# Kernel tuning notes

Measured on AMD Instinct MI355X. Metric: run time of the kernel, lower is better.

Reference implementation:

```python
import jax, jax.numpy as jnp
import numpy as np

N = 50000      # nodes
E = 800000     # edges (before self-loops)
F_IN = 128     # raw node feature dim
D = 500        # GCN_in_dim = gcn_dim = h_mlp_dim
T = 200000     # number of triplets


def setup_inputs() -> dict:
    key = jax.random.key(0)
    ks = jax.random.split(key, 13)
    s = 0.05
    return {
        "feats": jax.random.normal(ks[0], (N, F_IN), jnp.float32),
        "W_aff": jax.random.normal(ks[1], (F_IN, D), jnp.float32) * s,
        "b_aff": jax.random.normal(ks[2], (D,), jnp.float32) * s,
        "W_gcn": jax.random.normal(ks[3], (D, D), jnp.float32) * s,
        "b_gcn": jax.random.normal(ks[4], (D,), jnp.float32) * s,
        "W_pred_in": jax.random.normal(ks[5], (2 * D, D), jnp.float32) * s,
        "b_pred_in": jax.random.normal(ks[6], (D,), jnp.float32) * s,
        "W_pred_out": jax.random.normal(ks[7], (D, 1), jnp.float32) * s,
        "b_pred_out": jax.random.normal(ks[8], (1,), jnp.float32) * s,
        "src": jax.random.randint(ks[9], (E,), 0, N),
        "dst": jax.random.randint(ks[10], (E,), 0, N),
        "triplets": jax.random.randint(ks[11], (T, 3), 0, N),
    }


def reference(feats, W_aff, b_aff, W_gcn, b_gcn, W_pred_in, b_pred_in,
              W_pred_out, b_pred_out, src, dst, triplets):
    n = feats.shape[0]
    # LinearAffine (use_pre_linearAffine=True)
    x = feats @ W_aff + b_aff                      # [N, D]

    # dgl.add_self_loop
    loop = jnp.arange(n)
    s_idx = jnp.concatenate([src, loop])
    d_idx = jnp.concatenate([dst, loop])

    # GraphConv, norm='both', no edge weights, activation=None
    ones = jnp.ones(s_idx.shape[0], jnp.float32)
    out_deg = jax.ops.segment_sum(ones, s_idx, num_segments=n)
    in_deg = jax.ops.segment_sum(ones, d_idx, num_segments=n)
    norm_src = jnp.where(out_deg > 0, jax.lax.rsqrt(out_deg), 0.0)  # [N]
    norm_dst = jnp.where(in_deg > 0, jax.lax.rsqrt(in_deg), 0.0)    # [N]

    xw = x @ W_gcn                                  # [N, D]
    msg = xw[s_idx] * norm_src[s_idx, None]         # [E+N, D] gather
    agg = jax.ops.segment_sum(msg, d_idx, num_segments=n)  # scatter-add
    embedding = agg * norm_dst[:, None] + b_gcn     # [N, D]

    # triplet gather + MLP_edge_predictor (layer_num=2: cat->Linear->Linear)
    s_feat = embedding[triplets[:, 0]]              # [T, D]
    o_feat = embedding[triplets[:, 2]]              # [T, D]
    t = jnp.concatenate([s_feat, o_feat], axis=-1) @ W_pred_in + b_pred_in
    weights = t @ W_pred_out + b_pred_out           # [T, 1]
    return (weights, embedding)
```

## Files before the change

### kernel.cpp

```cpp
#include <hip/hip_runtime.h>


typedef float f32x4 __attribute__((ext_vector_type(4)));
typedef short s16x8 __attribute__((ext_vector_type(8)));

__device__ __forceinline__ unsigned short f2bf(float f) {
    unsigned u = __float_as_uint(f);
    unsigned r = (u + 0x7FFFu + ((u >> 16) & 1u)) >> 16;
    return (unsigned short)r;
}

__device__ __forceinline__ void async_ld16(const void* g, void* lds) {
    __builtin_amdgcn_global_load_lds(
        (const __attribute__((address_space(1))) unsigned int*)g,
        (__attribute__((address_space(3))) unsigned int*)lds,
        16, 0, 0);
}

__global__ __launch_bounds__(256) void init_kernel(
    unsigned* __restrict__ gpad, int nG,
    float* __restrict__ hpad, int nH, int* __restrict__ bh, int nB) {
    const int stride = gridDim.x * blockDim.x;
    const int i0 = blockIdx.x * blockDim.x + threadIdx.x;
    for (int i = i0; i < nG; i += stride) gpad[i] = 0u;
    for (int i = i0; i < nH; i += stride) hpad[i] = 0.f;
    for (int i = i0; i < nB; i += stride) bh[i] = 0;
}

__global__ __launch_bounds__(256) void hist2_kernel(
    const int* __restrict__ src, const int* __restrict__ dst,
    int* __restrict__ bhist_src, int* __restrict__ bhist_dst, int E) {
    __shared__ int lhs[256], lhd[256];
    lhs[threadIdx.x] = 0;
    lhd[threadIdx.x] = 0;
    __syncthreads();
    const int stride = gridDim.x * blockDim.x;
    for (int e = blockIdx.x * blockDim.x + threadIdx.x; e < E; e += stride) {
        atomicAdd(&lhs[src[e] >> 8], 1);
        atomicAdd(&lhd[dst[e] >> 8], 1);
    }
    __syncthreads();
    int cs = lhs[threadIdx.x], cd = lhd[threadIdx.x];
    if (cs > 0) atomicAdd(&bhist_src[threadIdx.x], cs);
    if (cd > 0) atomicAdd(&bhist_dst[threadIdx.x], cd);
}

__global__ void bscan2_kernel(const int* __restrict__ bhist_src, const int* __restrict__ bhist_dst,
                              int* __restrict__ sbbase, int* __restrict__ sbcursor,
                              int* __restrict__ dbbase, int* __restrict__ dbcursor,
                              int nbuk, int E) {
    __shared__ int sv[256];
    const int tid = threadIdx.x;

    int c = (tid < nbuk) ? bhist_src[tid] : 0;
    sv[tid] = c;
    __syncthreads();
    for (int st = 1; st < 256; st <<= 1) {
        int t = (tid >= st) ? sv[tid - st] : 0;
        __syncthreads();
        sv[tid] += t;
        __syncthreads();
    }
    if (tid < nbuk) { int ex = sv[tid] - c; sbbase[tid] = ex; sbcursor[tid] = ex; }
    if (tid == 0) sbbase[nbuk] = E;
    __syncthreads();

    c = (tid < nbuk) ? bhist_dst[tid] : 0;
    sv[tid] = c;
    __syncthreads();
    for (int st = 1; st < 256; st <<= 1) {
        int t = (tid >= st) ? sv[tid - st] : 0;
        __syncthreads();
        sv[tid] += t;
        __syncthreads();
    }
    if (tid < nbuk) { int ex = sv[tid] - c; dbbase[tid] = ex; dbcursor[tid] = ex; }
    if (tid == 0) dbbase[nbuk] = E;
}

#define PCH 4096
__global__ __launch_bounds__(256) void fused_partition_kernel(
    const int* __restrict__ src, const int* __restrict__ dst,
    int* __restrict__ dcursor, unsigned long long* __restrict__ pairs,
    int* __restrict__ scursor, int* __restrict__ ssorted,
    int E, int nbuk) {
    __shared__ int lhist[256];
    __shared__ int lbase[256];
    __shared__ int gbase[256];
    __shared__ int scanv[256];
    __shared__ unsigned long long lpair[PCH];
    __shared__ unsigned char lbid[PCH];

    const int tid = threadIdx.x;
    const int c0 = blockIdx.x * PCH;
    int cnt = E - c0; if (cnt > PCH) cnt = PCH;

    int dv[16], sv[16], rk[16];

    lhist[tid] = 0;
    __syncthreads();
#pragma unroll
    for (int q = 0; q < 16; ++q) {
        int e = c0 + q * 256 + tid;
        if (e < E) {
            int d = dst[e];
            dv[q] = d;
            sv[q] = src[e];
            rk[q] = atomicAdd(&lhist[d >> 8], 1);
        } else {
            dv[q] = -1;
            sv[q] = -1;
        }
    }
    __syncthreads();

    int c = lhist[tid];
    scanv[tid] = c;
    __syncthreads();
    for (int st = 1; st < 256; st <<= 1) {
        int t = (tid >= st) ? scanv[tid - st] : 0;
        __syncthreads();
        scanv[tid] += t;
        __syncthreads();
    }
    lbase[tid] = scanv[tid] - c;
    if (tid < nbuk && c > 0) gbase[tid] = atomicAdd(&dcursor[tid], c);
    __syncthreads();

#pragma unroll
    for (int q = 0; q < 16; ++q) {
        if (dv[q] >= 0) {
            int b = dv[q] >> 8;
            int slot = lbase[b] + rk[q];
            lpair[slot] = ((unsigned long long)(unsigned)dv[q] << 32) | (unsigned)sv[q];
            lbid[slot] = (unsigned char)b;
        }
    }
    __syncthreads();

    for (int i = tid; i < cnt; i += 256) {
        int b = lbid[i];
        pairs[(long)gbase[b] + (i - lbase[b])] = lpair[i];
    }
    __syncthreads();

    int* lval = (int*)lpair;
    lhist[tid] = 0;
    __syncthreads();
#pragma unroll
    for (int q = 0; q < 16; ++q) {
        if (sv[q] >= 0) rk[q] = atomicAdd(&lhist[sv[q] >> 8], 1);
    }
    __syncthreads();

    c = lhist[tid];
    scanv[tid] = c;
    __syncthreads();
    for (int st = 1; st < 256; st <<= 1) {
        int t = (tid >= st) ? scanv[tid - st] : 0;
        __syncthreads();
        scanv[tid] += t;
        __syncthreads();
    }
    lbase[tid] = scanv[tid] - c;
    if (tid < nbuk && c > 0) gbase[tid] = atomicAdd(&scursor[tid], c);
    __syncthreads();

#pragma unroll
    for (int q = 0; q < 16; ++q) {
        if (sv[q] >= 0) {
            int b = sv[q] >> 8;
            int slot = lbase[b] + rk[q];
            lval[slot] = sv[q];
            lbid[slot] = (unsigned char)b;
        }
    }
    __syncthreads();

    for (int i = tid; i < cnt; i += 256) {
        int b = lbid[i];
        ssorted[(long)gbase[b] + (i - lbase[b])] = lval[i];
    }
}

__global__ __launch_bounds__(256) void bucket_finalize_kernel(
    const unsigned long long* __restrict__ pairs, const int* __restrict__ dbbase,
    const int* __restrict__ ssorted, const int* __restrict__ sbbase,
    const float* __restrict__ feats,
    int* __restrict__ row_ptr, float* __restrict__ ndv,
    int* __restrict__ csr_src, float* __restrict__ ns,
    unsigned short* __restrict__ fs16, int N) {
    __shared__ int hist[256];
    __shared__ int scanv[256];
    __shared__ int lcur[256];
    __shared__ float nsv[256];
    const int tid = threadIdx.x;
    const int b = blockIdx.x;
    const int node = b * 256 + tid;

    const int e0 = dbbase[b], e1 = dbbase[b + 1];
    hist[tid] = 0;
    __syncthreads();
    for (int e = e0 + tid; e < e1; e += 256) {
        int d = (int)(pairs[e] >> 32);
        atomicAdd(&hist[d & 255], 1);
    }
    __syncthreads();

    int c = hist[tid];
    scanv[tid] = c;
    __syncthreads();
    for (int st = 1; st < 256; st <<= 1) {
        int t = (tid >= st) ? scanv[tid - st] : 0;
        __syncthreads();
        scanv[tid] += t;
        __syncthreads();
    }
    int excl = scanv[tid] - c;
    if (node < N) {
        row_ptr[node] = e0 + excl;
        ndv[node] = rsqrtf((float)(c + 1));
    }
    if (node == N) row_ptr[N] = e0 + excl;
    lcur[tid] = excl;
    __syncthreads();

    for (int e = e0 + tid; e < e1; e += 256) {
        unsigned long long pr = pairs[e];
        int d = (int)(pr >> 32);
        int r = atomicAdd(&lcur[d & 255], 1);
        csr_src[e0 + r] = (int)(pr & 0xFFFFFFFFu);
    }

    __syncthreads();
    hist[tid] = 0;
    __syncthreads();
    const int s0 = sbbase[b], s1 = sbbase[b + 1];
    for (int e = s0 + tid; e < s1; e += 256) atomicAdd(&hist[ssorted[e] & 255], 1);
    __syncthreads();
    float nsval = rsqrtf((float)(hist[tid] + 1));
    nsv[tid] = nsval;
    if (node < N) ns[node] = nsval;
    __syncthreads();

    for (int r0 = 0; r0 < 256; r0 += 16) {
        int r = r0 + (tid >> 4);
        int nn = b * 256 + r;
        if (nn >= N) break;
        int cq = (tid & 15) * 8;
        float s = nsv[r];
        const float* pf = feats + (long)nn * 128 + cq;
        float4 a = *reinterpret_cast<const float4*>(pf);
        float4 d2 = *reinterpret_cast<const float4*>(pf + 4);
        uint4 o;
        o.x = (unsigned)f2bf(a.x * s) | ((unsigned)f2bf(a.y * s) << 16);
        o.y = (unsigned)f2bf(a.z * s) | ((unsigned)f2bf(a.w * s) << 16);
        o.z = (unsigned)f2bf(d2.x * s) | ((unsigned)f2bf(d2.y * s) << 16);
        o.w = (unsigned)f2bf(d2.z * s) | ((unsigned)f2bf(d2.w * s) << 16);
        *reinterpret_cast<uint4*>(fs16 + (long)nn * 128 + cq) = o;
    }
}

__global__ __launch_bounds__(256) void dense_prep_kernel(
    const float* __restrict__ A, int lda,
    const float* __restrict__ B, int ldb,
    float* __restrict__ Cp, int ldc, int M, int Nn, int K,
    const float* __restrict__ b_aff, float* __restrict__ part,
    const float* __restrict__ Win, const float* __restrict__ wout,
    float* __restrict__ v,
    const float* __restrict__ b_in, const float* __restrict__ b_out,
    float* __restrict__ bdot,
    int D, int PD, int gxn, int gyn, int NBsg, int NBbc, int NBv, int nbper) {
    __shared__ __align__(16) float As[16][68];
    __shared__ __align__(16) float Bs[16][68];
    const int blk = blockIdx.x;
    const int tid = threadIdx.x;

    if (blk < NBsg) {
        const int gx = blk % gxn;
        const int gy = (blk / gxn) % gyn;
        const int gz = blk / (gxn * gyn);
        const int tx = tid & 15, ty = tid >> 4;
        const int row0 = gx * 64;
        const int col0 = gy * 64;
        const int kbeg = gz * 128;
        int kend = kbeg + 128; if (kend > K) kend = K;
        float* C = Cp + (long)gz * M * ldc;

        const int a_row = tid >> 2;
        const int a_k   = (tid & 3) * 4;
        const int b_k   = tid >> 4;
        const int b_c   = (tid & 15) * 4;

        float acc[4][4] = {};

        for (int k0 = kbeg; k0 < kend; k0 += 16) {
            float4 av = make_float4(0.f, 0.f, 0.f, 0.f);
            {
                int gr = row0 + a_row;
                int gk = k0 + a_k;
                if (gr < M) {
                    if (gk + 3 < kend) {
                        av = *reinterpret_cast<const float4*>(&A[(long)gr * lda + gk]);
                    } else {
                        float t0 = (gk + 0 < kend) ? A[(long)gr * lda + gk + 0] : 0.f;
                        float t1 = (gk + 1 < kend) ? A[(long)gr * lda + gk + 1] : 0.f;
                        float t2 = (gk + 2 < kend) ? A[(long)gr * lda + gk + 2] : 0.f;
                        float t3 = (gk + 3 < kend) ? A[(long)gr * lda + gk + 3] : 0.f;
                        av = make_float4(t0, t1, t2, t3);
                    }
                }
            }
            float4 bv = make_float4(0.f, 0.f, 0.f, 0.f);
            {
                int gk = k0 + b_k;
                int gc = col0 + b_c;
                if (gk < kend) {
                    if (gc + 3 < Nn) {
                        bv = *reinterpret_cast<const float4*>(&B[(long)gk * ldb + gc]);
                    } else {
                        float t0 = (gc + 0 < Nn) ? B[(long)gk * ldb + gc + 0] : 0.f;
                        float t1 = (gc + 1 < Nn) ? B[(long)gk * ldb + gc + 1] : 0.f;
                        float t2 = (gc + 2 < Nn) ? B[(long)gk * ldb + gc + 2] : 0.f;
                        float t3 = (gc + 3 < Nn) ? B[(long)gk * ldb + gc + 3] : 0.f;
                        bv = make_float4(t0, t1, t2, t3);
                    }
                }
            }
            __syncthreads();
            As[a_k + 0][a_row] = av.x;
            As[a_k + 1][a_row] = av.y;
            As[a_k + 2][a_row] = av.z;
            As[a_k + 3][a_row] = av.w;
            *reinterpret_cast<float4*>(&Bs[b_k][b_c]) = bv;
            __syncthreads();

#pragma unroll
            for (int k = 0; k < 16; ++k) {
                const float4 a = *reinterpret_cast<const float4*>(&As[k][ty * 4]);
                const float4 b2 = *reinterpret_cast<const float4*>(&Bs[k][tx * 4]);
                const float avv[4] = {a.x, a.y, a.z, a.w};
                const float bvv[4] = {b2.x, b2.y, b2.z, b2.w};
#pragma unroll
                for (int i = 0; i < 4; ++i)
#pragma unroll
                    for (int j = 0; j < 4; ++j)
                        acc[i][j] = fmaf(avv[i], bvv[j], acc[i][j]);
            }
        }

#pragma unroll
        for (int i = 0; i < 4; ++i) {
            int r = row0 + ty * 4 + i;
            if (r >= M) continue;
#pragma unroll
            for (int j = 0; j < 4; ++j) {
                int cc = col0 + tx * 4 + j;
                if (cc < Nn) C[(long)r * ldc + cc] = acc[i][j];
            }
        }
    } else if (blk < NBsg + NBbc) {
        int b2 = blk - NBsg;
        int nblk = b2 % nbper;
        int cch = b2 / nbper;
        int n = nblk * 256 + tid;
        if (n >= PD) return;
        float s = 0.f;
        if (n < D) {
            int k0 = cch * 8;
            int k1 = k0 + 8; if (k1 > D) k1 = D;
            for (int k = k0; k < k1; ++k) s = fmaf(b_aff[k], B[(long)k * ldb + n], s);
        }
        part[(long)cch * PD + n] = s;
    } else if (blk < NBsg + NBbc + NBv) {
        int k = (blk - NBsg - NBbc) * 4 + (tid >> 6);
        int lane = tid & 63;
        if (k >= 2 * D) return;
        float s = 0.f;
        for (int cc = lane; cc < D; cc += 64) s = fmaf(Win[(long)k * D + cc], wout[cc], s);
#pragma unroll
        for (int m = 32; m > 0; m >>= 1) s += __shfl_down(s, m);
        if (lane == 0) v[k] = s;
    } else {
        float* sm = &As[0][0];
        float s = 0.f;
        for (int cc = tid; cc < D; cc += 256) s = fmaf(b_in[cc], wout[cc], s);
        sm[tid] = s;
        __syncthreads();
        for (int st = 128; st > 0; st >>= 1) {
            if (tid < st) sm[tid] += sm[tid + st];
            __syncthreads();
        }
        if (tid == 0) bdot[0] = sm[0] + b_out[0];
    }
}

__global__ __launch_bounds__(256) void convBt_pad_kernel(
    const float* __restrict__ Wcp, unsigned short* __restrict__ Bt,
    const float* __restrict__ part, const float* __restrict__ b_gcn,
    const float* __restrict__ v, float* __restrict__ bcp,
    float* __restrict__ bgp, float* __restrict__ v1p, float* __restrict__ v2p,
    int D, int PD, int NC, int F, int nConvBlk) {
    const int b = blockIdx.x;
    const int tid = threadIdx.x;
    if (b < nConvBlk) {
        int idx = b * 256 + tid;
        if (idx >= PD * 16) return;
        int n = idx >> 4;
        int k8 = (idx & 15) * 8;
        uint4 o = make_uint4(0, 0, 0, 0);
        if (n < D) {
            unsigned short t[8];
            const long FD = (long)F * D;
#pragma unroll
            for (int q = 0; q < 8; ++q) {
                long off = (long)(k8 + q) * D + n;
                float val = Wcp[off] + Wcp[FD + off] + Wcp[2 * FD + off] + Wcp[3 * FD + off];
                t[q] = f2bf(val);
            }
            o.x = (unsigned)t[0] | ((unsigned)t[1] << 16);
            o.y = (unsigned)t[2] | ((unsigned)t[3] << 16);
            o.z = (unsigned)t[4] | ((unsigned)t[5] << 16);
            o.w = (unsigned)t[6] | ((unsigned)t[7] << 16);
        }
        *reinterpret_cast<uint4*>(Bt + (long)n * 128 + k8) = o;
    } else {
        int i = (b - nConvBlk) * 256 + tid;
        if (i < PD) {
            float s = 0.f;
            for (int c = 0; c < NC; ++c) s += part[(long)c * PD + i];
            bcp[i] = s;
            bgp[i] = (i < D) ? b_gcn[i] : 0.f;
            v1p[i] = (i < D) ? v[i] : 0.f;
            v2p[i] = (i < D) ? v[D + i] : 0.f;
        }
    }
}

__global__ __launch_bounds__(256) void gather_feats_kernel(
    const unsigned short* __restrict__ fs16, const int* __restrict__ csr_src,
    const int* __restrict__ row_ptr, const float* __restrict__ ns,
    unsigned short* __restrict__ g16, float* __restrict__ h, int N) {
    int d = blockIdx.x * 4 + (threadIdx.x >> 6);
    int lane = threadIdx.x & 63;
    if (d >= N) return;
    const int g = lane >> 4;
    const int fl = lane & 15;

    float a[8] = {0.f, 0.f, 0.f, 0.f, 0.f, 0.f, 0.f, 0.f};
    float hacc = 0.f;

    const int beg = row_ptr[d], end = row_ptr[d + 1];
    for (int j0 = beg; j0 < end; j0 += 64) {
        int cnt = end - j0;
        if (cnt > 64) cnt = 64;
        int s = (lane < cnt) ? csr_src[j0 + lane] : 0;
        if (lane < cnt) hacc += ns[s];
        for (int k = 0; k < cnt; k += 8) {
            int k0 = k + g, k1 = k + 4 + g;
            int i0 = __shfl(s, k0 & 63);
            int i1 = __shfl(s, k1 & 63);
            uint4 v0 = make_uint4(0u, 0u, 0u, 0u), v1 = make_uint4(0u, 0u, 0u, 0u);
            if (k0 < cnt) v0 = *reinterpret_cast<const uint4*>(fs16 + (long)i0 * 128 + fl * 8);
            if (k1 < cnt) v1 = *reinterpret_cast<const uint4*>(fs16 + (long)i1 * 128 + fl * 8);
            a[0] += __uint_as_float(v0.x << 16); a[1] += __uint_as_float(v0.x & 0xFFFF0000u);
            a[2] += __uint_as_float(v0.y << 16); a[3] += __uint_as_float(v0.y & 0xFFFF0000u);
            a[4] += __uint_as_float(v0.z << 16); a[5] += __uint_as_float(v0.z & 0xFFFF0000u);
            a[6] += __uint_as_float(v0.w << 16); a[7] += __uint_as_float(v0.w & 0xFFFF0000u);
            a[0] += __uint_as_float(v1.x << 16); a[1] += __uint_as_float(v1.x & 0xFFFF0000u);
            a[2] += __uint_as_float(v1.y << 16); a[3] += __uint_as_float(v1.y & 0xFFFF0000u);
            a[4] += __uint_as_float(v1.z << 16); a[5] += __uint_as_float(v1.z & 0xFFFF0000u);
            a[6] += __uint_as_float(v1.w << 16); a[7] += __uint_as_float(v1.w & 0xFFFF0000u);
        }
    }

#pragma unroll
    for (int r = 0; r < 8; ++r) {
        a[r] += __shfl_xor(a[r], 16);
        a[r] += __shfl_xor(a[r], 32);
    }
    {
        uint4 sv4 = *reinterpret_cast<const uint4*>(fs16 + (long)d * 128 + fl * 8);
        a[0] += __uint_as_float(sv4.x << 16); a[1] += __uint_as_float(sv4.x & 0xFFFF0000u);
        a[2] += __uint_as_float(sv4.y << 16); a[3] += __uint_as_float(sv4.y & 0xFFFF0000u);
        a[4] += __uint_as_float(sv4.z << 16); a[5] += __uint_as_float(sv4.z & 0xFFFF0000u);
        a[6] += __uint_as_float(sv4.w << 16); a[7] += __uint_as_float(sv4.w & 0xFFFF0000u);
    }
#pragma unroll
    for (int m = 32; m > 0; m >>= 1) hacc += __shfl_xor(hacc, m);
    if (lane == 0) h[d] = hacc + ns[d];
    if (lane < 16) {
        uint4 o;
        o.x = (unsigned)f2bf(a[0]) | ((unsigned)f2bf(a[1]) << 16);
        o.y = (unsigned)f2bf(a[2]) | ((unsigned)f2bf(a[3]) << 16);
        o.z = (unsigned)f2bf(a[4]) | ((unsigned)f2bf(a[5]) << 16);
        o.w = (unsigned)f2bf(a[6]) | ((unsigned)f2bf(a[7]) << 16);
        *reinterpret_cast<uint4*>(g16 + (long)d * 128 + fl * 8) = o;
    }
}

__global__ __launch_bounds__(256) void gcn_gemm_kernel(
    const unsigned short* __restrict__ g16, const unsigned short* __restrict__ Bt,
    const float* __restrict__ h, const float* __restrict__ nd,
    const float* __restrict__ bcp, const float* __restrict__ bgp,
    const float* __restrict__ v1p, const float* __restrict__ v2p,
    float* __restrict__ emb, float* __restrict__ u1, float* __restrict__ u2,
    int M, int D) {

    __shared__ __align__(16) unsigned short As[128 * 128];
    __shared__ __align__(16) unsigned short Bs[128 * 32];
    __shared__ float us1[128], us2[128];

    const int tid  = threadIdx.x;
    const int w    = tid >> 6;
    const int lane = tid & 63;
    const int row0 = blockIdx.x * 128;

    const int r0   = 2 * w * 16 + (lane >> 2);
    const int r1   = (2 * w + 1) * 16 + (lane >> 2);
    const int slot = lane & 3;
    const int c0   = slot ^ ((r0 >> 1) & 3);
    const int c1   = slot ^ ((r1 >> 1) & 3);

    const unsigned short* pA0 = g16 + (long)(row0 + r0) * 128 + c0 * 8;
    const unsigned short* pA1 = g16 + (long)(row0 + r1) * 128 + c1 * 8;

    unsigned short* dA0 = As + 2 * w * 512;
    unsigned short* dA1 = As + (2 * w + 1) * 512;
    unsigned short* dB0 = Bs + 2 * w * 512;
    unsigned short* dB1 = Bs + (2 * w + 1) * 512;

#pragma unroll
    for (int kc = 0; kc < 4; ++kc) {
        async_ld16(pA0 + kc * 32, dA0 + kc * 4096);
        async_ld16(pA1 + kc * 32, dA1 + kc * 4096);
    }

    if (tid < 128) { us1[tid] = 0.f; us2[tid] = 0.f; }

    const int wrow = (w & 1) * 64;
    const int wcol = (w >> 1) * 64;
    const int lm = lane & 15, q = lane >> 4;

    float usum1[4][4], usum2[4][4];
#pragma unroll
    for (int i = 0; i < 4; ++i)
#pragma unroll
        for (int r = 0; r < 4; ++r) { usum1[i][r] = 0.f; usum2[i][r] = 0.f; }

    for (int ct = 0; ct < 4; ++ct) {
        const int col0 = ct * 128;
        const unsigned short* pB0 = Bt + (long)(col0 + r0) * 128 + c0 * 8;
        const unsigned short* pB1 = Bt + (long)(col0 + r1) * 128 + c1 * 8;

        f32x4 acc[4][4];
#pragma unroll
        for (int i = 0; i < 4; ++i)
#pragma unroll
            for (int j = 0; j < 4; ++j) acc[i][j] = (f32x4)0.f;

        for (int kc = 0; kc < 4; ++kc) {
            async_ld16(pB0 + kc * 32, dB0);
            async_ld16(pB1 + kc * 32, dB1);
            __syncthreads();

            s16x8 af[4], bf[4];
#pragma unroll
            for (int i = 0; i < 4; ++i) {
                int r = wrow + i * 16 + lm;
                int cs = q ^ ((r >> 1) & 3);
                af[i] = *reinterpret_cast<const s16x8*>(As + kc * 4096 + r * 32 + cs * 8);
                int n = wcol + i * 16 + lm;
                int cs2 = q ^ ((n >> 1) & 3);
                bf[i] = *reinterpret_cast<const s16x8*>(Bs + n * 32 + cs2 * 8);
            }
#pragma unroll
            for (int i = 0; i < 4; ++i)
#pragma unroll
                for (int j = 0; j < 4; ++j)
                    acc[i][j] = __builtin_amdgcn_mfma_f32_16x16x32_bf16(af[i], bf[j], acc[i][j], 0, 0, 0);
            __syncthreads();
        }

        float bcv[4], bgv[4], w1v[4], w2v[4];
        int colv[4];
#pragma unroll
        for (int j = 0; j < 4; ++j) {
            int cc = col0 + wcol + j * 16 + lm;
            colv[j] = cc;
            bcv[j] = bcp[cc];
            bgv[j] = bgp[cc];
            w1v[j] = v1p[cc];
            w2v[j] = v2p[cc];
        }
#pragma unroll
        for (int i = 0; i < 4; ++i) {
#pragma unroll
            for (int reg = 0; reg < 4; ++reg) {
                int row = row0 + wrow + i * 16 + q * 4 + reg;
                float hb = h[row];
                float sc = (row < M) ? nd[row] : 0.f;
                float s1 = 0.f, s2 = 0.f;
#pragma unroll
                for (int j = 0; j < 4; ++j) {
                    float o = fmaf(sc, acc[i][j][reg] + hb * bcv[j], bgv[j]);
                    if (row < M && colv[j] < D) emb[(long)row * D + colv[j]] = o;
                    s1 = fmaf(o, w1v[j], s1);
                    s2 = fmaf(o, w2v[j], s2);
                }
                usum1[i][reg] += s1;
                usum2[i][reg] += s2;
            }
        }
    }

#pragma unroll
    for (int mask = 1; mask < 16; mask <<= 1)
#pragma unroll
        for (int i = 0; i < 4; ++i)
#pragma unroll
            for (int reg = 0; reg < 4; ++reg) {
                usum1[i][reg] += __shfl_xor(usum1[i][reg], mask);
                usum2[i][reg] += __shfl_xor(usum2[i][reg], mask);
            }
    if (lm == 0) {
#pragma unroll
        for (int i = 0; i < 4; ++i)
#pragma unroll
            for (int reg = 0; reg < 4; ++reg) {
                int lr = wrow + i * 16 + q * 4 + reg;
                atomicAdd(&us1[lr], usum1[i][reg]);
                atomicAdd(&us2[lr], usum2[i][reg]);
            }
    }
    __syncthreads();
    if (tid < 128) {
        int row = row0 + tid;
        if (row < M) {
            u1[row] = us1[tid];
            u2[row] = us2[tid];
        }
    }
}

__global__ void weights_kernel(const int* __restrict__ trip, const float* __restrict__ u1,
                               const float* __restrict__ u2, const float* __restrict__ bdot,
                               float* __restrict__ w, int T) {
    int r = blockIdx.x * blockDim.x + threadIdx.x;
    if (r < T) {
        int s = trip[(long)r * 3 + 0];
        int o = trip[(long)r * 3 + 2];
        w[r] = u1[s] + u2[o] + bdot[0];
    }
}


extern "C" void kernel_launch(void* const* d_in, const int* in_sizes, int n_in,
                              void* d_out, int out_size, void* d_ws, size_t ws_size,
                              hipStream_t stream) {
    const float* feats      = (const float*)d_in[0];
    const float* W_aff      = (const float*)d_in[1];
    const float* b_aff      = (const float*)d_in[2];
    const float* W_gcn      = (const float*)d_in[3];
    const float* b_gcn      = (const float*)d_in[4];
    const float* W_pred_in  = (const float*)d_in[5];
    const float* b_pred_in  = (const float*)d_in[6];
    const float* W_pred_out = (const float*)d_in[7];
    const float* b_pred_out = (const float*)d_in[8];
    const int*   src        = (const int*)d_in[9];
    const int*   dst        = (const int*)d_in[10];
    const int*   trip       = (const int*)d_in[11];

    const int D = in_sizes[2];
    const int F = in_sizes[1] / D;
    const int N = in_sizes[0] / F;
    const int E = in_sizes[9];
    const int T = in_sizes[11] / 3;

    const int PD = 512;
    const int GX = (N + 127) / 128;
    const int Mpad = GX * 128;
    const int NC = (D + 7) / 8;
    const int NBUK = (N >> 8) + 1;
    const int KS = 4;

    float* weights = (float*)d_out;
    float* emb     = (float*)d_out + T;

    char* p = (char*)d_ws;
    unsigned short* fs16 = (unsigned short*)p;  p += (size_t)N * 128 * 2;
    unsigned short* g16  = (unsigned short*)p;  p += (size_t)Mpad * 128 * 2;
    unsigned long long* pairs = (unsigned long long*)p; p += (size_t)E * 8;
    int* ssorted = (int*)p;  p += (size_t)E * 4;
    unsigned short* Bt   = (unsigned short*)p;  p += (size_t)PD * 128 * 2;
    float* Wcp  = (float*)p;  p += (size_t)KS * F * D * 4;
    float* bparts = (float*)p;  p += (size_t)64 * PD * 4;
    float* bcp  = (float*)p;  p += PD * 4;
    float* bgp  = (float*)p;  p += PD * 4;
    float* v1p  = (float*)p;  p += PD * 4;
    float* v2p  = (float*)p;  p += PD * 4;
    float* v    = (float*)p;  p += 1024 * 4;
    float* bdot = (float*)p;  p += 16;
    float* ns   = (float*)p;  p += (size_t)N * 4;
    float* nd   = (float*)p;  p += (size_t)N * 4;
    float* h    = (float*)p;  p += (size_t)Mpad * 4;
    float* u1   = (float*)p;  p += (size_t)N * 4;
    float* u2   = (float*)p;  p += (size_t)N * 4;
    int* bhist_src = (int*)p;  p += 256 * 4;
    int* bhist_dst = (int*)p;  p += 256 * 4;
    int* sbbase   = (int*)p;  p += 260 * 4;
    int* sbcursor = (int*)p;  p += 256 * 4;
    int* dbbase   = (int*)p;  p += 260 * 4;
    int* dbcursor = (int*)p;  p += 256 * 4;
    int* row_ptr = (int*)p;  p += (size_t)(N + 1) * 4;
    int* csr_src = (int*)p;  p += (size_t)E * 4;

    init_kernel<<<128, 256, 0, stream>>>(
        (unsigned*)(g16 + (size_t)N * 128), (Mpad - N) * 128 / 2,
        h + N, Mpad - N,
        bhist_src, 512);

    hist2_kernel<<<256, 256, 0, stream>>>(src, dst, bhist_src, bhist_dst, E);
    bscan2_kernel<<<1, 256, 0, stream>>>(bhist_src, bhist_dst, sbbase, sbcursor,
                                         dbbase, dbcursor, NBUK, E);
    fused_partition_kernel<<<(E + PCH - 1) / PCH, 256, 0, stream>>>(
        src, dst, dbcursor, pairs, sbcursor, ssorted, E, NBUK);
    bucket_finalize_kernel<<<NBUK, 256, 0, stream>>>(pairs, dbbase, ssorted, sbbase,
                                                     feats, row_ptr, nd, csr_src, ns,
                                                     fs16, N);

    {
        const int gxn = (F + 63) / 64;
        const int gyn = (D + 63) / 64;
        const int NBsg = gxn * gyn * KS;
        const int nbper = (PD + 255) / 256;
        const int NBbc = nbper * NC;
        const int NBv = (2 * D + 3) / 4;
        dense_prep_kernel<<<NBsg + NBbc + NBv + 1, 256, 0, stream>>>(
            W_aff, D, W_gcn, D, Wcp, D, F, D, D,
            b_aff, bparts, W_pred_in, W_pred_out, v,
            b_pred_in, b_pred_out, bdot,
            D, PD, gxn, gyn, NBsg, NBbc, NBv, nbper);
    }
    {
        const int nConvBlk = (PD * 16 + 255) / 256;
        const int nPadBlk = (PD + 255) / 256;
        convBt_pad_kernel<<<nConvBlk + nPadBlk, 256, 0, stream>>>(
            Wcp, Bt, bparts, b_gcn, v, bcp, bgp, v1p, v2p, D, PD, NC, F, nConvBlk);
    }

    gather_feats_kernel<<<(N + 3) / 4, 256, 0, stream>>>(fs16, csr_src, row_ptr, ns, g16, h, N);

    gcn_gemm_kernel<<<GX, 256, 0, stream>>>(g16, Bt, h, nd, bcp, bgp, v1p, v2p,
                                            emb, u1, u2, N, D);

    weights_kernel<<<(T + 255) / 256, 256, 0, stream>>>(trip, u1, u2, bdot, weights, T);
}
```

Measured before the change: 316.2 us.

## Split GCN GEMM over column tiles with a 2D grid and separate partial-sum fold

```diff
diff --git a/kernel.cpp b/kernel.cpp
--- a/kernel.cpp
+++ b/kernel.cpp
@@ -504,17 +504,17 @@
     const float* __restrict__ h, const float* __restrict__ nd,
     const float* __restrict__ bcp, const float* __restrict__ bgp,
     const float* __restrict__ v1p, const float* __restrict__ v2p,
-    float* __restrict__ emb, float* __restrict__ u1, float* __restrict__ u2,
-    int M, int D) {
-
-    __shared__ __align__(16) unsigned short As[128 * 128];
+    float* __restrict__ emb, float* __restrict__ u1part, float* __restrict__ u2part,
+    int M, int D, int Mpad) {
+
+    __shared__ __align__(16) unsigned short As[128 * 32];
     __shared__ __align__(16) unsigned short Bs[128 * 32];
-    __shared__ float us1[128], us2[128];
 
     const int tid  = threadIdx.x;
     const int w    = tid >> 6;
     const int lane = tid & 63;
     const int row0 = blockIdx.x * 128;
+    const int col0 = blockIdx.y * 128;
 
     const int r0   = 2 * w * 16 + (lane >> 2);
     const int r1   = (2 * w + 1) * 16 + (lane >> 2);
@@ -524,122 +524,116 @@
 
     const unsigned short* pA0 = g16 + (long)(row0 + r0) * 128 + c0 * 8;
     const unsigned short* pA1 = g16 + (long)(row0 + r1) * 128 + c1 * 8;
+    const unsigned short* pB0 = Bt + (long)(col0 + r0) * 128 + c0 * 8;
+    const unsigned short* pB1 = Bt + (long)(col0 + r1) * 128 + c1 * 8;
 
     unsigned short* dA0 = As + 2 * w * 512;
     unsigned short* dA1 = As + (2 * w + 1) * 512;
     unsigned short* dB0 = Bs + 2 * w * 512;
     unsigned short* dB1 = Bs + (2 * w + 1) * 512;
 
-#pragma unroll
-    for (int kc = 0; kc < 4; ++kc) {
-        async_ld16(pA0 + kc * 32, dA0 + kc * 4096);
-        async_ld16(pA1 + kc * 32, dA1 + kc * 4096);
-    }
-
-    if (tid < 128) { us1[tid] = 0.f; us2[tid] = 0.f; }
-
     const int wrow = (w & 1) * 64;
     const int wcol = (w >> 1) * 64;
     const int lm = lane & 15, q = lane >> 4;
-
-    float usum1[4][4], usum2[4][4];
+    const s16x8* pa[4];
+    const s16x8* pb[4];
+#pragma unroll
+    for (int i = 0; i < 4; ++i) {
+        int r = wrow + i * 16 + lm;
+        int cs = q ^ ((r >> 1) & 3);
+        pa[i] = reinterpret_cast<const s16x8*>(As + r * 32 + cs * 8);
+        int n = wcol + i * 16 + lm;
+        int cs2 = q ^ ((n >> 1) & 3);
+        pb[i] = reinterpret_cast<const s16x8*>(Bs + n * 32 + cs2 * 8);
+    }
+
+    f32x4 acc[4][4];
 #pragma unroll
     for (int i = 0; i < 4; ++i)
 #pragma unroll
-        for (int r = 0; r < 4; ++r) { usum1[i][r] = 0.f; usum2[i][r] = 0.f; }
-
-    for (int ct = 0; ct < 4; ++ct) {
-        const int col0 = ct * 128;
-        const unsigned short* pB0 = Bt + (long)(col0 + r0) * 128 + c0 * 8;
-        const unsigned short* pB1 = Bt + (long)(col0 + r1) * 128 + c1 * 8;
-
-        f32x4 acc[4][4];
+        for (int j = 0; j < 4; ++j) acc[i][j] = (f32x4)0.f;
+
+    for (int k0 = 0; k0 < 128; k0 += 32) {
+        async_ld16(pA0 + k0, dA0);
+        async_ld16(pA1 + k0, dA1);
+        async_ld16(pB0 + k0, dB0);
+        async_ld16(pB1 + k0, dB1);
+        __syncthreads();
+
+        s16x8 af[4], bf[4];
+#pragma unroll
+        for (int i = 0; i < 4; ++i) { af[i] = *pa[i]; bf[i] = *pb[i]; }
 #pragma unroll
         for (int i = 0; i < 4; ++i)
 #pragma unroll
-            for (int j = 0; j < 4; ++j) acc[i][j] = (f32x4)0.f;
-
-        for (int kc = 0; kc < 4; ++kc) {
-            async_ld16(pB0 + kc * 32, dB0);
-            async_ld16(pB1 + kc * 32, dB1);
-            __syncthreads();
-
-            s16x8 af[4], bf[4];
-#pragma unroll
-            for (int i = 0; i < 4; ++i) {
-                int r = wrow + i * 16 + lm;
-                int cs = q ^ ((r >> 1) & 3);
-                af[i] = *reinterpret_cast<const s16x8*>(As + kc * 4096 + r * 32 + cs * 8);
-                int n = wcol + i * 16 + lm;
-                int cs2 = q ^ ((n >> 1) & 3);
-                bf[i] = *reinterpret_cast<const s16x8*>(Bs + n * 32 + cs2 * 8);
+            for (int j = 0; j < 4; ++j)
+                acc[i][j] = __builtin_amdgcn_mfma_f32_16x16x32_bf16(af[i], bf[j], acc[i][j], 0, 0, 0);
+        __syncthreads();
+    }
+
+    float bcv[4], bgv[4], w1[4], w2[4];
+    int colv[4];
+#pragma unroll
+    for (int j = 0; j < 4; ++j) {
+        int c = col0 + wcol + j * 16 + lm;
+        colv[j] = c;
+        bcv[j] = bcp[c];
+        bgv[j] = bgp[c];
+        w1[j] = v1p[c];
+        w2[j] = v2p[c];
+    }
+
+    const int pb2 = blockIdx.y * 2 + (w >> 1);
+
+#pragma unroll
+    for (int i = 0; i < 4; ++i) {
+        float p1[4], p2[4];
+#pragma unroll
+        for (int reg = 0; reg < 4; ++reg) {
+            int row = row0 + wrow + i * 16 + q * 4 + reg;
+            float hb = h[row];
+            float sc = (row < M) ? nd[row] : 0.f;
+            float s1 = 0.f, s2 = 0.f;
+#pragma unroll
+            for (int j = 0; j < 4; ++j) {
+                float o = fmaf(sc, acc[i][j][reg] + hb * bcv[j], bgv[j]);
+                if (row < M && colv[j] < D) emb[(long)row * D + colv[j]] = o;
+                s1 = fmaf(o, w1[j], s1);
+                s2 = fmaf(o, w2[j], s2);
             }
-#pragma unroll
-            for (int i = 0; i < 4; ++i)
-#pragma unroll
-                for (int j = 0; j < 4; ++j)
-                    acc[i][j] = __builtin_amdgcn_mfma_f32_16x16x32_bf16(af[i], bf[j], acc[i][j], 0, 0, 0);
-            __syncthreads();
-        }
-
-        float bcv[4], bgv[4], w1v[4], w2v[4];
-        int colv[4];
-#pragma unroll
-        for (int j = 0; j < 4; ++j) {
-            int cc = col0 + wcol + j * 16 + lm;
-            colv[j] = cc;
-            bcv[j] = bcp[cc];
-            bgv[j] = bgp[cc];
-            w1v[j] = v1p[cc];
-            w2v[j] = v2p[cc];
-        }
-#pragma unroll
-        for (int i = 0; i < 4; ++i) {
+            p1[reg] = s1;
+            p2[reg] = s2;
+        }
+#pragma unroll
+        for (int mask = 1; mask < 16; mask <<= 1)
+#pragma unroll
+            for (int reg = 0; reg < 4; ++reg) {
+                p1[reg] += __shfl_xor(p1[reg], mask);
+                p2[reg] += __shfl_xor(p2[reg], mask);
+            }
+        if (lm == 0) {
 #pragma unroll
             for (int reg = 0; reg < 4; ++reg) {
                 int row = row0 + wrow + i * 16 + q * 4 + reg;
-                float hb = h[row];
-                float sc = (row < M) ? nd[row] : 0.f;
-                float s1 = 0.f, s2 = 0.f;
-#pragma unroll
-                for (int j = 0; j < 4; ++j) {
-                    float o = fmaf(sc, acc[i][j][reg] + hb * bcv[j], bgv[j]);
-                    if (row < M && colv[j] < D) emb[(long)row * D + colv[j]] = o;
-                    s1 = fmaf(o, w1v[j], s1);
-                    s2 = fmaf(o, w2v[j], s2);
-                }
-                usum1[i][reg] += s1;
-                usum2[i][reg] += s2;
+                u1part[(long)pb2 * Mpad + row] = p1[reg];
+                u2part[(long)pb2 * Mpad + row] = p2[reg];
             }
         }
     }
-
-#pragma unroll
-    for (int mask = 1; mask < 16; mask <<= 1)
-#pragma unroll
-        for (int i = 0; i < 4; ++i)
-#pragma unroll
-            for (int reg = 0; reg < 4; ++reg) {
-                usum1[i][reg] += __shfl_xor(usum1[i][reg], mask);
-                usum2[i][reg] += __shfl_xor(usum2[i][reg], mask);
-            }
-    if (lm == 0) {
-#pragma unroll
-        for (int i = 0; i < 4; ++i)
-#pragma unroll
-            for (int reg = 0; reg < 4; ++reg) {
-                int lr = wrow + i * 16 + q * 4 + reg;
-                atomicAdd(&us1[lr], usum1[i][reg]);
-                atomicAdd(&us2[lr], usum2[i][reg]);
-            }
-    }
-    __syncthreads();
-    if (tid < 128) {
-        int row = row0 + tid;
-        if (row < M) {
-            u1[row] = us1[tid];
-            u2[row] = us2[tid];
-        }
+}
+
+__global__ void ufold_kernel(const float* __restrict__ u1part, const float* __restrict__ u2part,
+                             float* __restrict__ u1, float* __restrict__ u2, int N, int Mpad) {
+    int i = blockIdx.x * blockDim.x + threadIdx.x;
+    if (i < N) {
+        float s1 = 0.f, s2 = 0.f;
+#pragma unroll
+        for (int pb = 0; pb < 8; ++pb) {
+            s1 += u1part[(long)pb * Mpad + i];
+            s2 += u2part[(long)pb * Mpad + i];
+        }
+        u1[i] = s1;
+        u2[i] = s2;
     }
 }
 
@@ -706,6 +700,8 @@
     float* h    = (float*)p;  p += (size_t)Mpad * 4;
     float* u1   = (float*)p;  p += (size_t)N * 4;
     float* u2   = (float*)p;  p += (size_t)N * 4;
+    float* u1part = (float*)p;  p += (size_t)8 * Mpad * 4;
+    float* u2part = (float*)p;  p += (size_t)8 * Mpad * 4;
     int* bhist_src = (int*)p;  p += 256 * 4;
     int* bhist_dst = (int*)p;  p += 256 * 4;
     int* sbbase   = (int*)p;  p += 260 * 4;
@@ -751,8 +747,12 @@
 
     gather_feats_kernel<<<(N + 3) / 4, 256, 0, stream>>>(fs16, csr_src, row_ptr, ns, g16, h, N);
 
-    gcn_gemm_kernel<<<GX, 256, 0, stream>>>(g16, Bt, h, nd, bcp, bgp, v1p, v2p,
-                                            emb, u1, u2, N, D);
-
+    {
+        dim3 grid(GX, PD / 128);
+        gcn_gemm_kernel<<<grid, 256, 0, stream>>>(g16, Bt, h, nd, bcp, bgp, v1p, v2p,
+                                                  emb, u1part, u2part, N, D, Mpad);
+    }
+
+    ufold_kernel<<<(N + 255) / 256, 256, 0, stream>>>(u1part, u2part, u1, u2, N, Mpad);
     weights_kernel<<<(T + 255) / 256, 256, 0, stream>>>(trip, u1, u2, bdot, weights, T);
 }
```

Measured after the change: 310.0 us. 1.02x faster.
